# Kernel optimization log

Hardware: AMD Instinct MI355X
Metric: run time of the kernel (lower is better)

Reference implementation:

```python
import jax, jax.numpy as jnp
import numpy as np

N = 30000          # nodes
DEG = 16           # in-degree per node
E = N * DEG        # edges per etype
T = 3              # edge types
IN = 128           # in_feats
HID = 256          # hidden_size
HEADS = 4
CLS = 2            # num_classes
NEG_SLOPE = 0.2    # DGL GATConv default


def setup_inputs() -> dict:
    key = jax.random.key(0)
    ks = jax.random.split(key, 14)
    s = lambda k, shape: (jax.random.normal(k, shape, jnp.float32) * 0.05)
    feat = jax.random.normal(ks[0], (N, IN), jnp.float32)
    src = jax.random.randint(ks[1], (T, E), 0, N)
    # every node gets exactly DEG incoming edges per etype (DGL forbids 0-in-degree)
    dst = jnp.tile(jnp.repeat(jnp.arange(N), DEG), (T, 1))
    D = HID // HEADS
    return {
        "feat": feat,
        "W0": s(ks[2], (T, IN, HID)),  "al0": s(ks[3], (T, HEADS, D)), "ar0": s(ks[4], (T, HEADS, D)), "b0": jnp.zeros((T, HID), jnp.float32),
        "W1": s(ks[5], (T, HID, HID)), "al1": s(ks[6], (T, HEADS, D)), "ar1": s(ks[7], (T, HEADS, D)), "b1": jnp.zeros((T, HID), jnp.float32),
        "W2": s(ks[8], (T, HID, CLS)), "al2": s(ks[9], (T, 1, CLS)),   "ar2": s(ks[10], (T, 1, CLS)), "b2": jnp.zeros((T, CLS), jnp.float32),
        "src": src, "dst": dst,
    }


def _gat(feat, W, al, ar, b, src, dst):
    """DGL GATConv: feat [n,F], W [F,H*D], al/ar [H,D], b [H*D] -> [n,H,D]."""
    n = feat.shape[0]
    H, D = al.shape
    h = (feat @ W).reshape(n, H, D)                      # projected features
    el = jnp.sum(h * al, axis=-1)                        # [n,H]
    er = jnp.sum(h * ar, axis=-1)                        # [n,H]
    e = jax.nn.leaky_relu(el[src] + er[dst], NEG_SLOPE)  # [E,H] edge scores
    # segment softmax over incoming edges of each dst node
    emax = jax.ops.segment_max(e, dst, num_segments=n)
    ex = jnp.exp(e - emax[dst])
    den = jax.ops.segment_sum(ex, dst, num_segments=n)
    alpha = ex / den[dst]                                # [E,H]
    out = jax.ops.segment_sum(h[src] * alpha[:, :, None], dst, num_segments=n)
    return out + b.reshape(H, D)


def _hetero(feat, W, al, ar, b, src, dst):
    # HeteroGraphConv(aggregate='mean') over T edge types on one node type
    outs = [_gat(feat, W[t], al[t], ar[t], b[t], src[t], dst[t]) for t in range(W.shape[0])]
    return jnp.mean(jnp.stack(outs, 0), axis=0)


def reference(feat, W0, al0, ar0, b0, W1, al1, ar1, b1, W2, al2, ar2, b2, src, dst):
    h = jax.nn.elu(_hetero(feat, W0, al0, ar0, b0, src, dst).reshape(N, -1))
    h = jax.nn.elu(_hetero(h, W1, al1, ar1, b1, src, dst).reshape(N, -1))
    logits = _hetero(h, W2, al2, ar2, b2, src, dst)      # [N,1,CLS]
    # faithful to F.softmax(logits[primary_ntype], dim=1): dim=1 is the size-1 head axis
    return logits, jax.nn.softmax(logits, axis=1)
```

## Files before the change

kernel.cpp:

```cpp
#include <hip/hip_runtime.h>
#include <hip/hip_bf16.h>
#include <hip/hip_fp8.h>
#include <math.h>

#define N_NODES 30000
#define DEG     16
#define NE      480000
#define NT      3
#define IN_F    128
#define HID_F   256
#define HEADS   4
#define DH      64
#define CLS     2
#define SLOPE   0.2f

#define NTILES      1875
#define NTILES_AL   1880
#define KC0         4
#define KC1         8

typedef __hip_bfloat16 bf16;
typedef __attribute__((ext_vector_type(8))) short short8;
typedef __attribute__((ext_vector_type(4))) float floatx4;

__device__ __forceinline__ float bf2f(short x) {
    unsigned int u = ((unsigned int)(unsigned short)x) << 16;
    float f;
    __builtin_memcpy(&f, &u, 4);
    return f;
}
__device__ __forceinline__ short f2bf_s(float x) {
    bf16 b = bf16(x);
    short s;
    __builtin_memcpy(&s, &b, 2);
    return s;
}

__device__ __forceinline__ void fp8x4_decode(unsigned int u, float* f) {
#if __has_builtin(__builtin_amdgcn_cvt_pk_f32_fp8)
    auto lo = __builtin_amdgcn_cvt_pk_f32_fp8((int)u, false);
    auto hi = __builtin_amdgcn_cvt_pk_f32_fp8((int)u, true);
    f[0] = lo[0]; f[1] = lo[1]; f[2] = hi[0]; f[3] = hi[1];
#else
#pragma unroll
    for (int j = 0; j < 4; j++) {
        __hip_fp8_e4m3 q;
        q.__x = (unsigned char)((u >> (8 * j)) & 0xff);
        f[j] = (float)q;
    }
#endif
}
__device__ __forceinline__ unsigned int fp8_encode4_u32(float v0, float v1,
                                                        float v2, float v3) {
#if __has_builtin(__builtin_amdgcn_cvt_pk_fp8_f32)
    int p01 = __builtin_amdgcn_cvt_pk_fp8_f32(v0, v1, 0, false);
    int p23 = __builtin_amdgcn_cvt_pk_fp8_f32(v2, v3, 0, false);
    return ((unsigned int)p01 & 0xffffu) | ((unsigned int)p23 << 16);
#else
    __hip_fp8_e4m3 q0(v0), q1(v1), q2(v2), q3(v3);
    return (unsigned int)q0.__x | ((unsigned int)q1.__x << 8) |
           ((unsigned int)q2.__x << 16) | ((unsigned int)q3.__x << 24);
#endif
}


#define APACK_THREADS (N_NODES * (IN_F / 8))
#define BP0_THREADS   (NT * 16 * KC0 * 64)
#define BP1_THREADS   (NT * 16 * KC1 * 64)
__global__ void prep(const float* __restrict__ feat, const float* __restrict__ W0,
                     const float* __restrict__ W1, short* __restrict__ Apack0,
                     short* __restrict__ Bpack0, short* __restrict__ Bpack1) {
    int g = blockIdx.x * 256 + threadIdx.x;
    if (g < APACK_THREADS) {
        int row = g >> 4, j8 = g & 15;
        int k0 = j8 * 8;
        const float* src = feat + (size_t)row * IN_F + k0;
        int ntile = row >> 4, C = k0 >> 5, quad = (k0 >> 3) & 3;
        int lane  = (row & 15) + 16 * quad;
        short* dst = Apack0 + ((size_t)(ntile * KC0 + C) * 64 + lane) * 8;
        short8 o;
#pragma unroll
        for (int j = 0; j < 8; j++) o[j] = f2bf_s(src[j]);
        *(short8*)dst = o;
        return;
    }
    g -= APACK_THREADS;
    if (g < BP0_THREADS) {
        int t = g / (16 * KC0 * 64), rem = g % (16 * KC0 * 64);
        int nt = rem / (KC0 * 64);
        int C  = (rem / 64) % KC0;
        int lane = rem & 63, l15 = lane & 15, quad = lane >> 4;
        int col = nt * 16 + l15, k0 = C * 32 + quad * 8;
        const float* src = W0 + (size_t)t * IN_F * HID_F + (size_t)k0 * HID_F + col;
        short* dst = Bpack0 + ((size_t)t * 16 * KC0 + nt * KC0 + C) * 512 + lane * 8;
        short8 o;
#pragma unroll
        for (int j = 0; j < 8; j++) o[j] = f2bf_s(src[(size_t)j * HID_F]);
        *(short8*)dst = o;
        return;
    }
    g -= BP0_THREADS;
    if (g < BP1_THREADS) {
        int t = g / (16 * KC1 * 64), rem = g % (16 * KC1 * 64);
        int nt = rem / (KC1 * 64);
        int C  = (rem / 64) % KC1;
        int lane = rem & 63, l15 = lane & 15, quad = lane >> 4;
        int col = nt * 16 + l15, k0 = C * 32 + quad * 8;
        const float* src = W1 + (size_t)t * HID_F * HID_F + (size_t)k0 * HID_F + col;
        short* dst = Bpack1 + ((size_t)t * 16 * KC1 + nt * KC1 + C) * 512 + lane * 8;
        short8 o;
#pragma unroll
        for (int j = 0; j < 8; j++) o[j] = f2bf_s(src[(size_t)j * HID_F]);
        *(short8*)dst = o;
    }
}

template <int K>
__global__ __launch_bounds__(256, 4) void gemm_proj(const short* __restrict__ Apack,
                                                    const short* __restrict__ Bpack,
                                                    const float* __restrict__ al,
                                                    const float* __restrict__ ar,
                                                    unsigned char* __restrict__ Hout,
                                                    float* __restrict__ el,
                                                    float* __restrict__ er) {
    const int KC = K / 32;
    int nh   = blockIdx.y;
    int t    = blockIdx.z;
    int tid  = threadIdx.x;
    int wave = tid >> 6, lane = tid & 63;
    int quad = lane >> 4, l15 = lane & 15;
    int e0   = blockIdx.x * 8 + wave * 2;

    const short* Ap0 = Apack + (size_t)(e0)     * KC * 512 + lane * 8;
    const short* Ap1 = Apack + (size_t)(e0 + 1) * KC * 512 + lane * 8;
    const short* Bp  = Bpack + ((size_t)t * 16 + nh * 8) * KC * 512 + lane * 8;
    unsigned char* Ht = Hout + (size_t)t * N_NODES * HID_F;

    floatx4 acc[8][2];
#pragma unroll
    for (int i = 0; i < 8; i++) {
        acc[i][0] = (floatx4){0.f, 0.f, 0.f, 0.f};
        acc[i][1] = (floatx4){0.f, 0.f, 0.f, 0.f};
    }

#pragma unroll
    for (int C = 0; C < KC; C++) {
        short8 xb0 = *(const short8*)(Ap0 + (size_t)C * 512);
        short8 xb1 = *(const short8*)(Ap1 + (size_t)C * 512);
#pragma unroll
        for (int nt = 0; nt < 8; nt++) {
            short8 wa = *(const short8*)(Bp + (size_t)(nt * KC + C) * 512);
            acc[nt][0] = __builtin_amdgcn_mfma_f32_16x16x32_bf16(wa, xb0, acc[nt][0], 0, 0, 0);
            acc[nt][1] = __builtin_amdgcn_mfma_f32_16x16x32_bf16(wa, xb1, acc[nt][1], 0, 0, 0);
        }
    }

#pragma unroll
    for (int e = 0; e < 2; e++) {
        int node = (e0 + e) * 16 + l15;
        bool ok  = node < N_NODES;
#pragma unroll
        for (int nt = 0; nt < 8; nt++) {
            unsigned int u = fp8_encode4_u32(acc[nt][e][0], acc[nt][e][1],
                                             acc[nt][e][2], acc[nt][e][3]);
            if (ok)
                *(unsigned int*)(Ht + (size_t)node * HID_F + (nh * 8 + nt) * 16 + quad * 4) = u;
        }
#pragma unroll
        for (int hl = 0; hl < 2; hl++) {
            int h = nh * 2 + hl;
            float pl = 0.f, pr = 0.f;
#pragma unroll
            for (int j = 0; j < 4; j++) {
                int nt = hl * 4 + j;
                int coff = t * HID_F + (nh * 8 + nt) * 16 + quad * 4;
                float4 av = *(const float4*)(al + coff);
                float4 rv = *(const float4*)(ar + coff);
                pl += acc[nt][e][0] * av.x + acc[nt][e][1] * av.y +
                      acc[nt][e][2] * av.z + acc[nt][e][3] * av.w;
                pr += acc[nt][e][0] * rv.x + acc[nt][e][1] * rv.y +
                      acc[nt][e][2] * rv.z + acc[nt][e][3] * rv.w;
            }
            pl += __shfl_xor(pl, 16); pl += __shfl_xor(pl, 32);
            pr += __shfl_xor(pr, 16); pr += __shfl_xor(pr, 32);
            if (lane < 16 && ok) {
                el[((size_t)t * N_NODES + node) * HEADS + h] = pl;
                er[((size_t)t * N_NODES + node) * HEADS + h] = pr;
            }
        }
    }
}

template <bool PACK>
__global__ __launch_bounds__(256, 4) void gat_agg(const unsigned char* __restrict__ Hproj,
                                                  const float* __restrict__ el,
                                                  const float* __restrict__ er,
                                                  const int* __restrict__ src,
                                                  const float* __restrict__ bias,
                                                  short* __restrict__ out) {
    int blk = blockIdx.x;
    int tid = threadIdx.x;
    __shared__ int   s_src[8][NT][DEG];
    __shared__ float s_w[8][NT][HEADS][DEG];

#pragma unroll
    for (int it = 0; it < 2; it++) {
        int j = it * 256 + tid;
        if (j < NT * 128) {
            int t = j / 128, k = j % 128;
            s_src[k >> 4][t][k & 15] = src[(size_t)t * NE + blk * 128 + k];
        }
    }
    __syncthreads();

    {
        int lane16 = tid & 15;
        int ubase  = tid >> 4;
#pragma unroll
        for (int it = 0; it < 6; it++) {
            int u = it * 16 + ubase;
            int g = u / 12, rem = u % 12;
            int t = rem >> 2, h = rem & 3;
            int n = blk * 8 + g;
            int s = s_src[g][t][lane16];
            float e = el[((size_t)t * N_NODES + s) * HEADS + h] +
                      er[((size_t)t * N_NODES + n) * HEADS + h];
            e = e > 0.f ? e : SLOPE * e;
            float m = e;
            m = fmaxf(m, __shfl_xor(m, 1));
            m = fmaxf(m, __shfl_xor(m, 2));
            m = fmaxf(m, __shfl_xor(m, 4));
            m = fmaxf(m, __shfl_xor(m, 8));
            float p = __expf(e - m);
            float ss = p;
            ss += __shfl_xor(ss, 1);
            ss += __shfl_xor(ss, 2);
            ss += __shfl_xor(ss, 4);
            ss += __shfl_xor(ss, 8);
            s_w[g][t][h][lane16] = p / ss;
        }
    }
    __syncthreads();

    int g = tid >> 5, c = tid & 31;
    int n = blk * 8 + g;
    int h = c >> 3;
    int col0 = c * 8;

    float acc[8];
#pragma unroll
    for (int j = 0; j < 8; j++) acc[j] = 0.f;

#pragma unroll
    for (int t = 0; t < NT; t++) {
        const unsigned char* Hh = Hproj + (size_t)t * N_NODES * HID_F;
        uint2 v[DEG];
#pragma unroll
        for (int i = 0; i < DEG; i++) {
            int s = s_src[g][t][i];
            v[i] = *(const uint2*)(Hh + (size_t)s * HID_F + col0);
        }
#pragma unroll
        for (int i = 0; i < DEG; i++) {
            float w = s_w[g][t][h][i];
            float f[8];
            fp8x4_decode(v[i].x, f);
            fp8x4_decode(v[i].y, f + 4);
#pragma unroll
            for (int j = 0; j < 8; j++) acc[j] += w * f[j];
        }
    }

    short8 o;
#pragma unroll
    for (int j = 0; j < 8; j++) {
        float bsum = bias[0 * HID_F + col0 + j] + bias[1 * HID_F + col0 + j] +
                     bias[2 * HID_F + col0 + j];
        float res = (acc[j] + bsum) * (1.f / 3.f);
        res = res > 0.f ? res : (__expf(res) - 1.f);
        o[j] = f2bf_s(res);
    }
    if (PACK) {
        int ntile = n >> 4, kc = c >> 2, quad = c & 3;
        int lane  = (n & 15) + 16 * quad;
        *(short8*)(out + ((size_t)(ntile * KC1 + kc) * 64 + lane) * 8) = o;
    } else {
        *(short8*)(out + (size_t)n * HID_F + col0) = o;
    }
}

__global__ __launch_bounds__(256) void proj2(const short* __restrict__ X,
                                             const float* __restrict__ W2,
                                             const float* __restrict__ al2,
                                             const float* __restrict__ ar2,
                                             float* __restrict__ p2,
                                             float* __restrict__ el2,
                                             float* __restrict__ er2) {
    int n    = blockIdx.x * 4 + (threadIdx.x >> 6);
    int lane = threadIdx.x & 63;
    const short* Xr = X + (size_t)n * HID_F + lane * 4;
    float x[4];
    x[0] = bf2f(Xr[0]); x[1] = bf2f(Xr[1]); x[2] = bf2f(Xr[2]); x[3] = bf2f(Xr[3]);
    float a[NT][CLS];
#pragma unroll
    for (int t = 0; t < NT; t++)
#pragma unroll
        for (int cc = 0; cc < CLS; cc++) {
            float v = 0.f;
#pragma unroll
            for (int j = 0; j < 4; j++)
                v += x[j] * W2[(size_t)t * HID_F * CLS + (lane * 4 + j) * CLS + cc];
#pragma unroll
            for (int off = 32; off; off >>= 1) v += __shfl_xor(v, off);
            a[t][cc] = v;
        }
    if (lane == 0) {
#pragma unroll
        for (int t = 0; t < NT; t++) {
            p2[((size_t)t * N_NODES + n) * CLS + 0] = a[t][0];
            p2[((size_t)t * N_NODES + n) * CLS + 1] = a[t][1];
            el2[(size_t)t * N_NODES + n] = a[t][0] * al2[t * CLS + 0] + a[t][1] * al2[t * CLS + 1];
            er2[(size_t)t * N_NODES + n] = a[t][0] * ar2[t * CLS + 0] + a[t][1] * ar2[t * CLS + 1];
        }
    }
}

__global__ void final_layer(const float* __restrict__ p2,
                            const float* __restrict__ el2,
                            const float* __restrict__ er2,
                            const int* __restrict__ src,
                            const float* __restrict__ b2,
                            float* __restrict__ out) {
    int n = blockIdx.x * 256 + threadIdx.x;
    if (n >= N_NODES) return;
    float l0 = 0.f, l1 = 0.f;
    for (int t = 0; t < NT; t++) {
        float erv = er2[(size_t)t * N_NODES + n];
        const int* sp = src + (size_t)t * NE + n * DEG;
        float ev[DEG];
        float m = -1e30f;
#pragma unroll
        for (int i = 0; i < DEG; i++) {
            int s   = sp[i];
            float e = el2[(size_t)t * N_NODES + s] + erv;
            e = e > 0.f ? e : SLOPE * e;
            ev[i] = e;
            m = fmaxf(m, e);
        }
        float den = 0.f, a0 = 0.f, a1 = 0.f;
#pragma unroll
        for (int i = 0; i < DEG; i++) {
            int s   = sp[i];
            float p = __expf(ev[i] - m);
            den += p;
            a0  += p * p2[((size_t)t * N_NODES + s) * CLS + 0];
            a1  += p * p2[((size_t)t * N_NODES + s) * CLS + 1];
        }
        l0 += a0 / den + b2[t * CLS + 0];
        l1 += a1 / den + b2[t * CLS + 1];
    }
    l0 *= (1.f / 3.f);
    l1 *= (1.f / 3.f);
    out[(size_t)n * CLS + 0] = l0;
    out[(size_t)n * CLS + 1] = l1;
    float* out2 = out + (size_t)N_NODES * CLS;
    out2[(size_t)n * CLS + 0] = 1.0f;
    out2[(size_t)n * CLS + 1] = 1.0f;
}

extern "C" void kernel_launch(void* const* d_in, const int* in_sizes, int n_in,
                              void* d_out, int out_size, void* d_ws, size_t ws_size,
                              hipStream_t stream) {
    const float* feat = (const float*)d_in[0];
    const float* W0   = (const float*)d_in[1];
    const float* al0  = (const float*)d_in[2];
    const float* ar0  = (const float*)d_in[3];
    const float* b0   = (const float*)d_in[4];
    const float* W1   = (const float*)d_in[5];
    const float* al1  = (const float*)d_in[6];
    const float* ar1  = (const float*)d_in[7];
    const float* b1   = (const float*)d_in[8];
    const float* W2   = (const float*)d_in[9];
    const float* al2  = (const float*)d_in[10];
    const float* ar2  = (const float*)d_in[11];
    const float* b2   = (const float*)d_in[12];
    const int*   src  = (const int*)d_in[13];

    char* w = (char*)d_ws;
    auto alloc = [&](size_t bytes) {
        char* p = w;
        w += (bytes + 255) & ~(size_t)255;
        return p;
    };
    short* Apack0 = (short*)alloc((size_t)NTILES_AL * KC0 * 512 * 2);
    short* Apack1 = (short*)alloc((size_t)NTILES_AL * KC1 * 512 * 2);
    short* Bpack0 = (short*)alloc((size_t)NT * 16 * KC0 * 512 * 2);
    short* Bpack1 = (short*)alloc((size_t)NT * 16 * KC1 * 512 * 2);
    unsigned char* Hproj = (unsigned char*)alloc((size_t)NT * N_NODES * HID_F);
    short* h2    = (short*)alloc((size_t)N_NODES * HID_F * 2);
    float* el    = (float*)alloc((size_t)NT * N_NODES * HEADS * 4);
    float* er    = (float*)alloc((size_t)NT * N_NODES * HEADS * 4);
    float* p2    = (float*)alloc((size_t)NT * N_NODES * CLS * 4);
    float* el2   = (float*)alloc((size_t)NT * N_NODES * 4);
    float* er2   = (float*)alloc((size_t)NT * N_NODES * 4);

    int prep_total = APACK_THREADS + BP0_THREADS + BP1_THREADS;
    prep<<<(prep_total + 255) / 256, 256, 0, stream>>>(feat, W0, W1, Apack0,
                                                       Bpack0, Bpack1);

    dim3 ggrid((NTILES + 7) / 8, 2, NT);

    gemm_proj<IN_F><<<ggrid, 256, 0, stream>>>(Apack0, Bpack0, al0, ar0, Hproj, el, er);
    gat_agg<true><<<N_NODES / 8, 256, 0, stream>>>(Hproj, el, er, src, b0, Apack1);

    gemm_proj<HID_F><<<ggrid, 256, 0, stream>>>(Apack1, Bpack1, al1, ar1, Hproj, el, er);
    gat_agg<false><<<N_NODES / 8, 256, 0, stream>>>(Hproj, el, er, src, b1, h2);

    proj2<<<dim3(N_NODES / 4), 256, 0, stream>>>(h2, W2, al2, ar2, p2, el2, er2);
    final_layer<<<(N_NODES + 255) / 256, 256, 0, stream>>>(p2, el2, er2, src, b2,
                                                           (float*)d_out);
}
```

Measured before the change: 323.4 us.

## Widen gat_agg gathers to 16-byte loads and process 16 nodes per block

The aggregation kernel now handles 16 nodes per block with 16 threads per node, so each thread gathers 16 fp8 features as one uint4 load instead of 8 bytes. The fp8 decode feeds packed two-wide float FMAs, and the 16 edge loads are split into two batches of 8 to limit register pressure. Launch bounds are raised to 8 blocks per CU, and the packed output layout is recomputed for the new thread mapping. The intent is fewer, wider memory transactions and less per-node setup, at the cost of fewer threads in flight per node and more shared memory per block.

Result: no change. 324.2 us (+0.2%).

```diff
diff --git a/kernel.cpp b/kernel.cpp
--- a/kernel.cpp
+++ b/kernel.cpp
@@ -22,6 +22,7 @@
 typedef __hip_bfloat16 bf16;
 typedef __attribute__((ext_vector_type(8))) short short8;
 typedef __attribute__((ext_vector_type(4))) float floatx4;
+typedef __attribute__((ext_vector_type(2))) float f32x2;
 
 __device__ __forceinline__ float bf2f(short x) {
     unsigned int u = ((unsigned int)(unsigned short)x) << 16;
@@ -36,18 +37,24 @@
     return s;
 }
 
-__device__ __forceinline__ void fp8x4_decode(unsigned int u, float* f) {
+__device__ __forceinline__ f32x2 fp8_lo(unsigned int u) {
 #if __has_builtin(__builtin_amdgcn_cvt_pk_f32_fp8)
-    auto lo = __builtin_amdgcn_cvt_pk_f32_fp8((int)u, false);
-    auto hi = __builtin_amdgcn_cvt_pk_f32_fp8((int)u, true);
-    f[0] = lo[0]; f[1] = lo[1]; f[2] = hi[0]; f[3] = hi[1];
+    return __builtin_amdgcn_cvt_pk_f32_fp8((int)u, false);
 #else
-#pragma unroll
-    for (int j = 0; j < 4; j++) {
-        __hip_fp8_e4m3 q;
-        q.__x = (unsigned char)((u >> (8 * j)) & 0xff);
-        f[j] = (float)q;
-    }
+    __hip_fp8_e4m3 q0, q1;
+    q0.__x = (unsigned char)(u & 0xff);
+    q1.__x = (unsigned char)((u >> 8) & 0xff);
+    return (f32x2){(float)q0, (float)q1};
+#endif
+}
+__device__ __forceinline__ f32x2 fp8_hi(unsigned int u) {
+#if __has_builtin(__builtin_amdgcn_cvt_pk_f32_fp8)
+    return __builtin_amdgcn_cvt_pk_f32_fp8((int)u, true);
+#else
+    __hip_fp8_e4m3 q2, q3;
+    q2.__x = (unsigned char)((u >> 16) & 0xff);
+    q3.__x = (unsigned char)((u >> 24) & 0xff);
+    return (f32x2){(float)q2, (float)q3};
 #endif
 }
 __device__ __forceinline__ unsigned int fp8_encode4_u32(float v0, float v1,
@@ -192,7 +199,7 @@
 }
 
 template <bool PACK>
-__global__ __launch_bounds__(256, 4) void gat_agg(const unsigned char* __restrict__ Hproj,
+__global__ __launch_bounds__(256, 8) void gat_agg(const unsigned char* __restrict__ Hproj,
                                                   const float* __restrict__ el,
                                                   const float* __restrict__ er,
                                                   const int* __restrict__ src,
@@ -200,16 +207,13 @@
                                                   short* __restrict__ out) {
     int blk = blockIdx.x;
     int tid = threadIdx.x;
-    __shared__ int   s_src[8][NT][DEG];
-    __shared__ float s_w[8][NT][HEADS][DEG];
-
-#pragma unroll
-    for (int it = 0; it < 2; it++) {
-        int j = it * 256 + tid;
-        if (j < NT * 128) {
-            int t = j / 128, k = j % 128;
-            s_src[k >> 4][t][k & 15] = src[(size_t)t * NE + blk * 128 + k];
-        }
+    __shared__ __align__(16) int   s_src[16][NT][DEG];
+    __shared__ __align__(16) float s_w[16][NT][HEADS][DEG];
+
+#pragma unroll
+    for (int t = 0; t < NT; t++) {
+        int j = tid;
+        s_src[j >> 4][t][j & 15] = src[(size_t)t * NE + blk * 256 + j];
     }
     __syncthreads();
 
@@ -217,11 +221,11 @@
         int lane16 = tid & 15;
         int ubase  = tid >> 4;
 #pragma unroll
-        for (int it = 0; it < 6; it++) {
+        for (int it = 0; it < 12; it++) {
             int u = it * 16 + ubase;
             int g = u / 12, rem = u % 12;
             int t = rem >> 2, h = rem & 3;
-            int n = blk * 8 + g;
+            int n = blk * 16 + g;
             int s = s_src[g][t][lane16];
             float e = el[((size_t)t * N_NODES + s) * HEADS + h] +
                       er[((size_t)t * N_NODES + n) * HEADS + h];
@@ -242,50 +246,75 @@
     }
     __syncthreads();
 
-    int g = tid >> 5, c = tid & 31;
-    int n = blk * 8 + g;
-    int h = c >> 3;
-    int col0 = c * 8;
-
-    float acc[8];
-#pragma unroll
-    for (int j = 0; j < 8; j++) acc[j] = 0.f;
+    int g = tid >> 4, c = tid & 15;
+    int n = blk * 16 + g;
+    int h = c >> 2;
+    int col0 = c * 16;
+
+    f32x2 acc2[8];
+#pragma unroll
+    for (int k = 0; k < 8; k++) acc2[k] = (f32x2){0.f, 0.f};
+
+    const uint4* Hb = (const uint4*)Hproj;
+    unsigned cu = (unsigned)c;
 
 #pragma unroll
     for (int t = 0; t < NT; t++) {
-        const unsigned char* Hh = Hproj + (size_t)t * N_NODES * HID_F;
-        uint2 v[DEG];
-#pragma unroll
-        for (int i = 0; i < DEG; i++) {
-            int s = s_src[g][t][i];
-            v[i] = *(const uint2*)(Hh + (size_t)s * HID_F + col0);
-        }
-#pragma unroll
-        for (int i = 0; i < DEG; i++) {
-            float w = s_w[g][t][h][i];
-            float f[8];
-            fp8x4_decode(v[i].x, f);
-            fp8x4_decode(v[i].y, f + 4);
-#pragma unroll
-            for (int j = 0; j < 8; j++) acc[j] += w * f[j];
-        }
-    }
-
-    short8 o;
+        const unsigned tb = (unsigned)t * (N_NODES * 16u);
+        const float* wp = s_w[g][t][h];
+#pragma unroll
+        for (int half = 0; half < 2; half++) {
+            uint4 v[8];
+#pragma unroll
+            for (int i = 0; i < 8; i++) {
+                int s = s_src[g][t][half * 8 + i];
+                v[i] = Hb[tb + (unsigned)s * 16u + cu];
+            }
+#pragma unroll
+            for (int i = 0; i < 8; i++) {
+                float wsc = wp[half * 8 + i];
+                f32x2 w2 = (f32x2){wsc, wsc};
+                acc2[0] += w2 * fp8_lo(v[i].x);
+                acc2[1] += w2 * fp8_hi(v[i].x);
+                acc2[2] += w2 * fp8_lo(v[i].y);
+                acc2[3] += w2 * fp8_hi(v[i].y);
+                acc2[4] += w2 * fp8_lo(v[i].z);
+                acc2[5] += w2 * fp8_hi(v[i].z);
+                acc2[6] += w2 * fp8_lo(v[i].w);
+                acc2[7] += w2 * fp8_hi(v[i].w);
+            }
+        }
+    }
+
+    short8 o0, o1;
 #pragma unroll
     for (int j = 0; j < 8; j++) {
+        float av = acc2[j >> 1][j & 1];
         float bsum = bias[0 * HID_F + col0 + j] + bias[1 * HID_F + col0 + j] +
                      bias[2 * HID_F + col0 + j];
-        float res = (acc[j] + bsum) * (1.f / 3.f);
+        float res = (av + bsum) * (1.f / 3.f);
         res = res > 0.f ? res : (__expf(res) - 1.f);
-        o[j] = f2bf_s(res);
+        o0[j] = f2bf_s(res);
+    }
+#pragma unroll
+    for (int j = 0; j < 8; j++) {
+        float av = acc2[4 + (j >> 1)][j & 1];
+        int cj = col0 + 8 + j;
+        float bsum = bias[0 * HID_F + cj] + bias[1 * HID_F + cj] +
+                     bias[2 * HID_F + cj];
+        float res = (av + bsum) * (1.f / 3.f);
+        res = res > 0.f ? res : (__expf(res) - 1.f);
+        o1[j] = f2bf_s(res);
     }
     if (PACK) {
-        int ntile = n >> 4, kc = c >> 2, quad = c & 3;
-        int lane  = (n & 15) + 16 * quad;
-        *(short8*)(out + ((size_t)(ntile * KC1 + kc) * 64 + lane) * 8) = o;
+        int C = c >> 1;
+        int lane0 = g + 16 * ((2 * c) & 3);
+        int lane1 = g + 16 * ((2 * c + 1) & 3);
+        *(short8*)(out + ((size_t)(blk * KC1 + C) * 64 + lane0) * 8) = o0;
+        *(short8*)(out + ((size_t)(blk * KC1 + C) * 64 + lane1) * 8) = o1;
     } else {
-        *(short8*)(out + (size_t)n * HID_F + col0) = o;
+        *(short8*)(out + (size_t)n * HID_F + col0) = o0;
+        *(short8*)(out + (size_t)n * HID_F + col0 + 8) = o1;
     }
 }
 
@@ -411,10 +440,10 @@
     dim3 ggrid((NTILES + 7) / 8, 2, NT);
 
     gemm_proj<IN_F><<<ggrid, 256, 0, stream>>>(Apack0, Bpack0, al0, ar0, Hproj, el, er);
-    gat_agg<true><<<N_NODES / 8, 256, 0, stream>>>(Hproj, el, er, src, b0, Apack1);
+    gat_agg<true><<<N_NODES / 16, 256, 0, stream>>>(Hproj, el, er, src, b0, Apack1);
 
     gemm_proj<HID_F><<<ggrid, 256, 0, stream>>>(Apack1, Bpack1, al1, ar1, Hproj, el, er);
-    gat_agg<false><<<N_NODES / 8, 256, 0, stream>>>(Hproj, el, er, src, b1, h2);
+    gat_agg<false><<<N_NODES / 16, 256, 0, stream>>>(Hproj, el, er, src, b1, h2);
 
     proj2<<<dim3(N_NODES / 4), 256, 0, stream>>>(h2, W2, al2, ar2, p2, el2, er2);
     final_layer<<<(N_NODES + 255) / 256, 256, 0, stream>>>(p2, el2, er2, src, b2,
```
